# Performance work log

Hardware: AMD Instinct MI355X
Metric: run time of the kernel (lower is better)

## Reference

```python
import jax, jax.numpy as jnp
import numpy as np

B, S, E = 2, 2048, 1024
H = 1344            # hidden_dim = ceil(1.3*1024/64)*64
NH = 4              # mLSTM heads
DH = H // NH        # 336
K = 4               # causal conv kernel size
NPH = H // 4        # headwise proj heads (qkv_proj_blocksize=4)
PD = H // NPH       # per-head proj dim = 4
EPS = 1e-6


def setup_inputs() -> dict:
    key = jax.random.key(0)
    ks = jax.random.split(key, 10)
    s_in = jnp.sqrt(2.0 / (5 * E))    # small_init(E)
    s_pd = jnp.sqrt(2.0 / (5 * PD))   # small_init per-head dim
    return {
        "x": jax.random.normal(ks[0], (B, S, E), jnp.float32),
        "W_up": jax.random.normal(ks[1], (E, 2 * H), jnp.float32) * s_in,
        "conv_k": jax.random.normal(ks[2], (K, 1, H), jnp.float32) * jnp.sqrt(2.0 / K),  # depthwise, WIO layout
        "conv_b": jnp.zeros((H,), jnp.float32),
        "Wq": jax.random.normal(ks[3], (NPH, PD, PD), jnp.float32) * s_pd,
        "Wk": jax.random.normal(ks[4], (NPH, PD, PD), jnp.float32) * s_pd,
        "Wv": jax.random.normal(ks[5], (NPH, PD, PD), jnp.float32) * s_pd,
        "W_ig": jax.random.normal(ks[6], (3 * H, NH), jnp.float32) * 0.01,
        "b_ig": jax.random.normal(ks[7], (NH,), jnp.float32) * 0.1,
        "W_fg": jax.random.normal(ks[8], (3 * H, NH), jnp.float32) * 0.01,
        "b_fg": jnp.linspace(3.0, 6.0, NH, dtype=jnp.float32),
        "ln_w": jnp.ones((H,), jnp.float32),
        "skip": jnp.ones((H,), jnp.float32),
        "W_down": jax.random.normal(ks[9], (H, E), jnp.float32) * (2.0 / 12 / np.sqrt(H)),
    }


def _headwise(x, W):
    # LinearHeadwiseExpand: block-diagonal projection over NPH heads of size PD
    xh = x.reshape(B, S, NPH, PD)
    return jnp.einsum('bshd,hdo->bsho', xh, W).reshape(B, S, H)


def _mlstm_cell(q, k, v, ig, fg):
    # parallel stabilized mLSTM; q,k,v: (B,NH,S,DH); ig,fg: (B,NH,S)
    logf = jax.nn.log_sigmoid(fg)
    c = jnp.cumsum(logf, axis=-1)                         # (B,NH,S)
    logfmat = c[..., :, None] - c[..., None, :]           # (B,NH,S,S) cumulative forget decay
    mask = jnp.tril(jnp.ones((S, S), bool))               # causal mask
    log_D = jnp.where(mask, logfmat, -jnp.inf) + ig[..., None, :]
    m = jnp.max(log_D, axis=-1, keepdims=True)            # rowwise stabilizer
    D = jnp.exp(log_D - m)
    qk = jnp.einsum('bnsd,bntd->bnst', q, k) * (DH ** -0.5)
    C = qk * D
    n = jnp.maximum(jnp.abs(jnp.sum(C, axis=-1, keepdims=True)), jnp.exp(-m))
    return jnp.einsum('bnst,bntd->bnsd', C / (n + EPS), v)


def reference(x, W_up, conv_k, conv_b, Wq, Wk, Wv, W_ig, b_ig, W_fg, b_fg, ln_w, skip, W_down):
    x_inner = x @ W_up                                    # (B,S,2H)
    x_m, z = jnp.split(x_inner, 2, axis=-1)
    # depthwise causal conv1d
    xp = jnp.pad(x_m, ((0, 0), (K - 1, 0), (0, 0)))
    xc = jax.lax.conv_general_dilated(
        xp, conv_k, (1,), 'VALID',
        dimension_numbers=('NWC', 'WIO', 'NWC'),
        feature_group_count=H) + conv_b
    act = jax.nn.silu(xc)
    q = _headwise(act, Wq)
    k = _headwise(act, Wk)
    v = _headwise(x_m, Wv)
    gin = jnp.concatenate([q, k, v], axis=-1)             # (B,S,3H)
    ig = jnp.transpose(gin @ W_ig + b_ig, (0, 2, 1))      # (B,NH,S)
    fg = jnp.transpose(gin @ W_fg + b_fg, (0, 2, 1))
    qh = jnp.transpose(q.reshape(B, S, NH, DH), (0, 2, 1, 3))
    kh = jnp.transpose(k.reshape(B, S, NH, DH), (0, 2, 1, 3))
    vh = jnp.transpose(v.reshape(B, S, NH, DH), (0, 2, 1, 3))
    h = _mlstm_cell(qh, kh, vh, ig, fg)                   # (B,NH,S,DH)
    # multi-head layernorm (per-head groupnorm over DH, scale only)
    mu = jnp.mean(h, axis=-1, keepdims=True)
    var = jnp.var(h, axis=-1, keepdims=True)
    hn = (h - mu) * jax.lax.rsqrt(var + 1e-5) * ln_w.reshape(NH, 1, DH)
    h_out = jnp.transpose(hn, (0, 2, 1, 3)).reshape(B, S, H)
    h_state = (h_out + skip * act) * jax.nn.silu(z)
    return h_state @ W_down
```

## Files before the change

### kernel.cpp

```cpp
#include <hip/hip_runtime.h>
#include <cmath>

#define DI __device__ __forceinline__

constexpr int B_=2, S_=2048, E_=1024, H_=1344, NH_=4, DH_=336;
constexpr int BS_=B_*S_, H2_=2*H_;
constexpr int NG_=B_*NH_*S_;

constexpr size_t N_X=(size_t)BS_*E_;
constexpr size_t N_WUP=(size_t)E_*H2_;
constexpr size_t N_WDN=(size_t)H_*E_;
constexpr size_t N_BSH=(size_t)BS_*H_;
constexpr size_t N_BSH2=(size_t)BS_*H2_;
constexpr size_t N_WH=5376, N_WG=16128, N_CK=4*H_;

constexpr size_t O_IGB = 64;
constexpr size_t O_LOGF= O_IGB + NG_;
constexpr size_t O_AB  = O_LOGF+ NG_;
constexpr size_t O_MB  = O_AB  + NG_;
constexpr size_t O_MTB = O_MB  + NG_;
constexpr size_t O_CK  = O_MTB + NG_;
constexpr size_t O_CB  = O_CK  + N_CK;
constexpr size_t O_WQ  = O_CB  + H_;
constexpr size_t O_WK  = O_WQ  + N_WH;
constexpr size_t O_WV  = O_WK  + N_WH;
constexpr size_t O_WIG = O_WV  + N_WH;
constexpr size_t O_BIG = O_WIG + N_WG;
constexpr size_t O_WFG = O_BIG + 16;
constexpr size_t O_BFG = O_WFG + N_WG;
constexpr size_t O_LNW = O_BFG + 16;
constexpr size_t O_SKP = O_LNW + H_;
constexpr size_t O_FX  = O_SKP + H_;
constexpr size_t O_FWUP= O_FX  + N_X;
constexpr size_t O_FWDN= O_FWUP+ N_WUP;
constexpr size_t O_XIN = O_FWDN+ N_WDN;
constexpr size_t O_ACT = O_XIN + N_BSH2;
constexpr size_t O_QB  = O_ACT + N_BSH;
constexpr size_t O_KB  = O_QB  + N_BSH;
constexpr size_t O_VB  = O_KB  + N_BSH;
constexpr size_t O_HOUT= O_VB  + N_BSH;

constexpr size_t KSPLIT_SHORTS=(size_t)8*128*11*64*8;
constexpr size_t VT_SHORTS=(size_t)8*64*22*64*8;

typedef __attribute__((ext_vector_type(8))) short bf16x8;
typedef __attribute__((ext_vector_type(4))) float f32x4;

DI float bf2f(unsigned int u){union{unsigned int i;float f;}v;v.i=(u&0xffffu)<<16;return v.f;}
DI unsigned short f2bf(float f){union{float f;unsigned int i;}v;v.f=f;unsigned int x=v.i;
  return (unsigned short)((x+0x7fffu+((x>>16)&1u))>>16);}
DI float siluf(float x){return x/(1.f+expf(-x));}
DI float logsigf(float x){return (x>=0.f)?-log1pf(expf(-x)):x-log1pf(expf(x));}
DI void load4(const float* p, float* d){float4 v=*reinterpret_cast<const float4*>(p);
  d[0]=v.x;d[1]=v.y;d[2]=v.z;d[3]=v.w;}

__global__ __launch_bounds__(256) void detect_k(const unsigned short* __restrict__ xraw,
                                                int* __restrict__ flag){
  __shared__ int cnt_s;
  if(threadIdx.x==0) cnt_s=0;
  __syncthreads();
  int c=0;
  for(int i=threadIdx.x;i<2048;i+=256){
    const unsigned e=(xraw[i]>>7)&0xFFu;
    if(e>=0x90u) c++;
  }
  atomicAdd(&cnt_s,c);
  __syncthreads();
  if(threadIdx.x==0) *flag=(cnt_s>16)?0:1;
}

__global__ __launch_bounds__(256) void convert_k(const void* __restrict__ src,
                                                 float* __restrict__ dst,int n,
                                                 const int* __restrict__ flag){
  const int i=blockIdx.x*256+threadIdx.x;
  if(i>=n) return;
  if(*flag) dst[i]=bf2f(((const unsigned short*)src)[i]);
  else      dst[i]=((const float*)src)[i];
}

__global__ __launch_bounds__(256) void aprep_k(const void* __restrict__ src,
                                               const int* __restrict__ flag,
                                               int kcn,int ldk,int total,
                                               unsigned short* __restrict__ hi,
                                               unsigned short* __restrict__ lo){
  const int slot=blockIdx.x*256+threadIdx.x;
  if(slot>=total) return;
  const int l=slot&63, rest=slot>>6;
  const int kc=rest%kcn, mt=rest/kcn;
  const int row=mt*16+(l&15), k0=kc*32+(l>>4)*8;
  const int fl=flag?*flag:0;
  float v[8];
  if(fl){
    const unsigned short* s=(const unsigned short*)src+(size_t)row*ldk+k0;
    const uint4 u=*reinterpret_cast<const uint4*>(s);
    v[0]=bf2f(u.x);v[1]=bf2f(u.x>>16);v[2]=bf2f(u.y);v[3]=bf2f(u.y>>16);
    v[4]=bf2f(u.z);v[5]=bf2f(u.z>>16);v[6]=bf2f(u.w);v[7]=bf2f(u.w>>16);
  }else{
    const float* s=(const float*)src+(size_t)row*ldk+k0;
    load4(s,v); load4(s+4,v+4);
  }
  unsigned short h8[8], l8[8];
#pragma unroll
  for(int j=0;j<8;j++){ h8[j]=f2bf(v[j]); l8[j]=f2bf(v[j]-bf2f(h8[j])); }
  uint4 ph,pl;
  ph.x=(unsigned)h8[0]|((unsigned)h8[1]<<16); ph.y=(unsigned)h8[2]|((unsigned)h8[3]<<16);
  ph.z=(unsigned)h8[4]|((unsigned)h8[5]<<16); ph.w=(unsigned)h8[6]|((unsigned)h8[7]<<16);
  pl.x=(unsigned)l8[0]|((unsigned)l8[1]<<16); pl.y=(unsigned)l8[2]|((unsigned)l8[3]<<16);
  pl.z=(unsigned)l8[4]|((unsigned)l8[5]<<16); pl.w=(unsigned)l8[6]|((unsigned)l8[7]<<16);
  *reinterpret_cast<uint4*>(&hi[(size_t)slot*8])=ph;
  *reinterpret_cast<uint4*>(&lo[(size_t)slot*8])=pl;
}

__global__ __launch_bounds__(256) void bprep_k(const void* __restrict__ src,
                                               const int* __restrict__ flag,
                                               int kcn,int ldn,int total,
                                               unsigned short* __restrict__ hi,
                                               unsigned short* __restrict__ lo){
  const int slot=blockIdx.x*256+threadIdx.x;
  if(slot>=total) return;
  const int l=slot&63, rest=slot>>6;
  const int kc=rest%kcn, nt=rest/kcn;
  const int col=nt*16+(l&15), row0=kc*32+(l>>4)*8;
  const int fl=flag?*flag:0;
  float v[8];
  if(fl){
    const unsigned short* s=(const unsigned short*)src;
#pragma unroll
    for(int j=0;j<8;j++) v[j]=bf2f(s[(size_t)(row0+j)*ldn+col]);
  }else{
    const float* s=(const float*)src;
#pragma unroll
    for(int j=0;j<8;j++) v[j]=s[(size_t)(row0+j)*ldn+col];
  }
  unsigned short h8[8], l8[8];
#pragma unroll
  for(int j=0;j<8;j++){ h8[j]=f2bf(v[j]); l8[j]=f2bf(v[j]-bf2f(h8[j])); }
  uint4 ph,pl;
  ph.x=(unsigned)h8[0]|((unsigned)h8[1]<<16); ph.y=(unsigned)h8[2]|((unsigned)h8[3]<<16);
  ph.z=(unsigned)h8[4]|((unsigned)h8[5]<<16); ph.w=(unsigned)h8[6]|((unsigned)h8[7]<<16);
  pl.x=(unsigned)l8[0]|((unsigned)l8[1]<<16); pl.y=(unsigned)l8[2]|((unsigned)l8[3]<<16);
  pl.z=(unsigned)l8[4]|((unsigned)l8[5]<<16); pl.w=(unsigned)l8[6]|((unsigned)l8[7]<<16);
  *reinterpret_cast<uint4*>(&hi[(size_t)slot*8])=ph;
  *reinterpret_cast<uint4*>(&lo[(size_t)slot*8])=pl;
}

__global__ __launch_bounds__(256) void gemm_mfma_k(
    const unsigned short* __restrict__ Ahi, const unsigned short* __restrict__ Alo,
    const unsigned short* __restrict__ Bhi, const unsigned short* __restrict__ Blo,
    void* __restrict__ C, const int* __restrict__ flag, int kcn, int ldc){
  const int t=threadIdx.x, w=t>>6, l=t&63, lm=l&15, quad=l>>4;
  const int bn=blockIdx.x*64, bm=blockIdx.y*128;
  const int mt0=(bm>>4)+w, mt1=mt0+4;
  const size_t a0=((size_t)mt0*kcn)*512+(size_t)l*8;
  const size_t a1=((size_t)mt1*kcn)*512+(size_t)l*8;
  const size_t b0=((size_t)(bn>>4)*kcn)*512+(size_t)l*8;
  f32x4 acc[2][4];
#pragma unroll
  for(int g=0;g<2;g++)
#pragma unroll
    for(int nt=0;nt<4;nt++) acc[g][nt]={0.f,0.f,0.f,0.f};
  for(int kc=0;kc<kcn;kc++){
    const bf16x8 ah0=*reinterpret_cast<const bf16x8*>(&Ahi[a0+(size_t)kc*512]);
    const bf16x8 al0=*reinterpret_cast<const bf16x8*>(&Alo[a0+(size_t)kc*512]);
    const bf16x8 ah1=*reinterpret_cast<const bf16x8*>(&Ahi[a1+(size_t)kc*512]);
    const bf16x8 al1=*reinterpret_cast<const bf16x8*>(&Alo[a1+(size_t)kc*512]);
#pragma unroll
    for(int nt=0;nt<4;nt++){
      const size_t bo=b0+((size_t)nt*kcn+kc)*512;
      const bf16x8 bh=*reinterpret_cast<const bf16x8*>(&Bhi[bo]);
      const bf16x8 bl=*reinterpret_cast<const bf16x8*>(&Blo[bo]);
      acc[0][nt]=__builtin_amdgcn_mfma_f32_16x16x32_bf16(ah0,bh,acc[0][nt],0,0,0);
      acc[0][nt]=__builtin_amdgcn_mfma_f32_16x16x32_bf16(al0,bh,acc[0][nt],0,0,0);
      acc[0][nt]=__builtin_amdgcn_mfma_f32_16x16x32_bf16(ah0,bl,acc[0][nt],0,0,0);
      acc[1][nt]=__builtin_amdgcn_mfma_f32_16x16x32_bf16(ah1,bh,acc[1][nt],0,0,0);
      acc[1][nt]=__builtin_amdgcn_mfma_f32_16x16x32_bf16(al1,bh,acc[1][nt],0,0,0);
      acc[1][nt]=__builtin_amdgcn_mfma_f32_16x16x32_bf16(ah1,bl,acc[1][nt],0,0,0);
    }
  }
  const int bf=flag?*flag:0;
#pragma unroll
  for(int g=0;g<2;g++)
#pragma unroll
    for(int nt=0;nt<4;nt++)
#pragma unroll
      for(int r=0;r<4;r++){
        const size_t idx=(size_t)(bm+g*64+w*16+quad*4+r)*ldc+bn+nt*16+lm;
        if(bf) ((unsigned short*)C)[idx]=f2bf(acc[g][nt][r]);
        else   ((float*)C)[idx]=acc[g][nt][r];
      }
}

__global__ __launch_bounds__(256) void conv_act_k(const float* __restrict__ xin,
                                                  const float* __restrict__ ck,
                                                  const float* __restrict__ cb,
                                                  float* __restrict__ act){
  const int i=blockIdx.x*256+threadIdx.x;
  if(i>=(int)N_BSH) return;
  const int bs=i/H_, h=i-bs*H_;
  const int b=bs/S_, s=bs-b*S_;
  float xc=cb[h];
#pragma unroll
  for(int w=0;w<4;w++){
    const int sr=s-3+w;
    if(sr>=0) xc+=xin[(size_t)(b*S_+sr)*H2_+h]*ck[w*H_+h];
  }
  act[(size_t)bs*H_+h]=siluf(xc);
}

__global__ __launch_bounds__(256) void qkv_k(const float* __restrict__ act,
                                             const float* __restrict__ xin,
                                             const float* __restrict__ Wq,
                                             const float* __restrict__ Wk,
                                             const float* __restrict__ Wv,
                                             float* __restrict__ qb,float* __restrict__ kb,
                                             float* __restrict__ vb){
  const int i=blockIdx.x*256+threadIdx.x;
  if(i>=(int)N_BSH) return;
  const int bs=i/H_, h=i-bs*H_;
  const int b=bs/S_, s=bs-b*S_;
  const int ph=h>>2, o=h&3, base=ph*4;
  float q=0.f,k=0.f,v=0.f;
#pragma unroll
  for(int d=0;d<4;d++){
    const float a=act[(size_t)bs*H_+base+d];
    const float x=xin[(size_t)bs*H2_+base+d];
    q+=a*Wq[ph*16+d*4+o];
    k+=a*Wk[ph*16+d*4+o];
    v+=x*Wv[ph*16+d*4+o];
  }
  const int nh=h/DH_, dh=h-nh*DH_;
  const size_t off=((size_t)(b*NH_+nh)*S_+s)*DH_+dh;
  qb[off]=q; kb[off]=k; vb[off]=v;
}

__global__ __launch_bounds__(256) void gates2_k(const float* __restrict__ qb,
                                                const float* __restrict__ kb,
                                                const float* __restrict__ vb,
                                                const float* __restrict__ Wig,
                                                const float* __restrict__ big,
                                                const float* __restrict__ Wfg,
                                                const float* __restrict__ bfg,
                                                float* __restrict__ igb,
                                                float* __restrict__ logfb){
  const int wid=(blockIdx.x*256+threadIdx.x)>>6;
  const int l=threadIdx.x&63;
  if(wid>=BS_) return;
  const int b=wid>>11, s=wid&2047;
  float aI0=0.f,aI1=0.f,aI2=0.f,aI3=0.f;
  float aF0=0.f,aF1=0.f,aF2=0.f,aF3=0.f;
  for(int nh=0;nh<NH_;nh++){
    const size_t rb=((size_t)(b*NH_+nh)*S_+s)*DH_;
    const int hb=nh*DH_;
    for(int dh=l;dh<DH_;dh+=64){
      const int h=hb+dh;
      const float q=qb[rb+dh], k=kb[rb+dh], v=vb[rb+dh];
      const float4 wiq=*reinterpret_cast<const float4*>(&Wig[(size_t)h*4]);
      const float4 wik=*reinterpret_cast<const float4*>(&Wig[(size_t)(H_+h)*4]);
      const float4 wiv=*reinterpret_cast<const float4*>(&Wig[(size_t)(2*H_+h)*4]);
      const float4 wfq=*reinterpret_cast<const float4*>(&Wfg[(size_t)h*4]);
      const float4 wfk=*reinterpret_cast<const float4*>(&Wfg[(size_t)(H_+h)*4]);
      const float4 wfv=*reinterpret_cast<const float4*>(&Wfg[(size_t)(2*H_+h)*4]);
      aI0+=q*wiq.x+k*wik.x+v*wiv.x;
      aI1+=q*wiq.y+k*wik.y+v*wiv.y;
      aI2+=q*wiq.z+k*wik.z+v*wiv.z;
      aI3+=q*wiq.w+k*wik.w+v*wiv.w;
      aF0+=q*wfq.x+k*wfk.x+v*wfv.x;
      aF1+=q*wfq.y+k*wfk.y+v*wfv.y;
      aF2+=q*wfq.z+k*wfk.z+v*wfv.z;
      aF3+=q*wfq.w+k*wfk.w+v*wfv.w;
    }
  }
#pragma unroll
  for(int m=1;m<64;m<<=1){
    aI0+=__shfl_xor(aI0,m); aI1+=__shfl_xor(aI1,m);
    aI2+=__shfl_xor(aI2,m); aI3+=__shfl_xor(aI3,m);
    aF0+=__shfl_xor(aF0,m); aF1+=__shfl_xor(aF1,m);
    aF2+=__shfl_xor(aF2,m); aF3+=__shfl_xor(aF3,m);
  }
  if(l==0){
    const size_t o0=(size_t)(b*NH_+0)*S_+s;
    const size_t o1=(size_t)(b*NH_+1)*S_+s;
    const size_t o2=(size_t)(b*NH_+2)*S_+s;
    const size_t o3=(size_t)(b*NH_+3)*S_+s;
    igb[o0]=aI0+big[0]; igb[o1]=aI1+big[1];
    igb[o2]=aI2+big[2]; igb[o3]=aI3+big[3];
    logfb[o0]=logsigf(aF0+bfg[0]); logfb[o1]=logsigf(aF1+bfg[1]);
    logfb[o2]=logsigf(aF2+bfg[2]); logfb[o3]=logsigf(aF3+bfg[3]);
  }
}

__global__ __launch_bounds__(256) void kprep_k(const float* __restrict__ kb,
                                               unsigned short* __restrict__ khi,
                                               unsigned short* __restrict__ klo){
  const int blk=blockIdx.x;
  const int head=blk>>7, tt=blk&127;
  const size_t obase=(size_t)blk*11*512;
  for(int slot=threadIdx.x; slot<704; slot+=256){
    const int dc=slot>>6, ll=slot&63, quad=ll>>4, lm=ll&15;
    const int tg=tt*16+lm, dbase=dc*32+quad*8;
    float v[8];
    if(dbase<336){
      load4(&kb[((size_t)head*S_+tg)*DH_+dbase],v);
      load4(&kb[((size_t)head*S_+tg)*DH_+dbase+4],v+4);
    } else { for(int j=0;j<8;j++) v[j]=0.f; }
    unsigned short hi8[8], lo8[8];
#pragma unroll
    for(int j=0;j<8;j++){
      hi8[j]=f2bf(v[j]);
      lo8[j]=f2bf(v[j]-bf2f(hi8[j]));
    }
    const size_t o=obase+(size_t)(dc*64+ll)*8;
    uint4 ph, pl;
    ph.x=(unsigned)hi8[0]|((unsigned)hi8[1]<<16); ph.y=(unsigned)hi8[2]|((unsigned)hi8[3]<<16);
    ph.z=(unsigned)hi8[4]|((unsigned)hi8[5]<<16); ph.w=(unsigned)hi8[6]|((unsigned)hi8[7]<<16);
    pl.x=(unsigned)lo8[0]|((unsigned)lo8[1]<<16); pl.y=(unsigned)lo8[2]|((unsigned)lo8[3]<<16);
    pl.z=(unsigned)lo8[4]|((unsigned)lo8[5]<<16); pl.w=(unsigned)lo8[6]|((unsigned)lo8[7]<<16);
    *reinterpret_cast<uint4*>(&khi[o])=ph;
    *reinterpret_cast<uint4*>(&klo[o])=pl;
  }
}

__global__ __launch_bounds__(256) void vprep_k(const float* __restrict__ vb,
                                               unsigned short* __restrict__ vTf){
  const int blk=blockIdx.x;
  const int head=blk>>6, tc=blk&63;
  const size_t obase=(size_t)blk*22*512;
  for(int slot=threadIdx.x; slot<1408; slot+=256){
    const int ntg=slot>>6, ll=slot&63, quad=ll>>4, lm=ll&15;
    const int n=ntg*16+lm, t0=tc*32+quad*8;
    unsigned short h8[8];
#pragma unroll
    for(int j=0;j<8;j++){
      float val;
      if(n<336)       val=vb[((size_t)head*S_+t0+j)*DH_+n];
      else if(n==336) val=1.f;
      else            val=0.f;
      h8[j]=f2bf(val);
    }
    uint4 pk;
    pk.x=(unsigned)h8[0]|((unsigned)h8[1]<<16); pk.y=(unsigned)h8[2]|((unsigned)h8[3]<<16);
    pk.z=(unsigned)h8[4]|((unsigned)h8[5]<<16); pk.w=(unsigned)h8[6]|((unsigned)h8[7]<<16);
    *reinterpret_cast<uint4*>(&vTf[obase+(size_t)(ntg*64+ll)*8])=pk;
  }
}

__global__ __launch_bounds__(256) void scan_k(const float* __restrict__ igb,
                                              const float* __restrict__ logfb,
                                              float* __restrict__ ab,float* __restrict__ Mb,
                                              float* __restrict__ mtb){
  const int head=blockIdx.x, t=threadIdx.x;
  __shared__ float sh[256];
  const float* lf=logfb+(size_t)head*S_;
  const float* ig=igb+(size_t)head*S_;
  float lc[8];
  float run=0.f;
#pragma unroll
  for(int i=0;i<8;i++){ run+=lf[t*8+i]; lc[i]=run; }
  sh[t]=run;
  for(int st=1;st<256;st<<=1){
    __syncthreads();
    const float v=(t>=st)?sh[t-st]:0.f;
    __syncthreads();
    sh[t]+=v;
  }
  __syncthreads();
  const float off=(t==0)?0.f:sh[t-1];
  __syncthreads();
  float av[8],mv[8],cv[8];
  float mrun=-1e30f;
#pragma unroll
  for(int i=0;i<8;i++){
    cv[i]=off+lc[i];
    av[i]=ig[t*8+i]-cv[i];
    mrun=fmaxf(mrun,av[i]);
    mv[i]=mrun;
  }
  sh[t]=mrun;
  for(int st=1;st<256;st<<=1){
    __syncthreads();
    const float v=(t>=st)?sh[t-st]:-1e30f;
    __syncthreads();
    sh[t]=fmaxf(sh[t],v);
  }
  __syncthreads();
  const float moff=(t==0)?-1e30f:sh[t-1];
#pragma unroll
  for(int i=0;i<8;i++){
    const float Mi=fmaxf(moff,mv[i]);
    const size_t j=(size_t)head*S_+t*8+i;
    ab[j]=av[i]; Mb[j]=Mi; mtb[j]=cv[i]+Mi;
  }
}

__global__ __launch_bounds__(512,1) void mlstm6_k(
    const float* __restrict__ qb, const unsigned short* __restrict__ khi,
    const unsigned short* __restrict__ klo, const unsigned short* __restrict__ vTf,
    const float* __restrict__ ab, const float* __restrict__ Mb,
    float* __restrict__ part, float* __restrict__ rsum){
  const int bid=blockIdx.x;
  const int head=bid&7;
  const int rest=bid>>3;
  const int pairI=rest&7, seg=rest>>3;
  const int t=threadIdx.x, w=t>>6, l=t&63, lm=l&15, quad=l>>4;

  __shared__ short KV[2][66*512];
  __shared__ short Sc[8][16][40];

  const size_t hb=(size_t)head*S_;
  const float scale=0.05455447256f;

  const int sbA=pairI, sbB=15-pairI;
  const int nA=pairI+1, nTot=17;

  bf16x8 qh[11], ql[11];
  f32x4 accO[22];
  float Mr[4];
  int ws0=sbA*128+w*16;

  auto loadQ=[&](int ws0_){
    const float* qrow=qb+(hb+ws0_+lm)*DH_;
#pragma unroll
    for(int dc=0;dc<11;dc++){
      const int dbase=dc*32+quad*8;
      float v[8];
      if(dbase<336){ load4(qrow+dbase,v); load4(qrow+dbase+4,v+4); }
      else { for(int j=0;j<8;j++) v[j]=0.f; }
#pragma unroll
      for(int j=0;j<8;j++){
        const unsigned short h=f2bf(v[j]);
        qh[dc][j]=(short)h;
        ql[dc][j]=(short)f2bf(v[j]-bf2f(h));
      }
    }
#pragma unroll
    for(int r=0;r<4;r++) Mr[r]=Mb[hb+ws0_+quad*4+r];
#pragma unroll
    for(int n=0;n<22;n++) accO[n]={0.f,0.f,0.f,0.f};
  };

  auto itemC=[&](int i)->int{
    return (i<nA)? (seg+4*i) : (seg+4*(i-nA));
  };

  auto stage=[&](int buf,int c){
    const size_t kbase=(((size_t)head*128+(size_t)(2*c))*11)*512+(size_t)l*8;
    const size_t vbase=(((size_t)head*64+(size_t)c)*22)*512+(size_t)l*8;
#pragma unroll
    for(int j=0;j<9;j++){
      const int tr=w+8*j;
      if(tr<66){
        const unsigned short* src;
        if(tr<22)      src=&khi[kbase+(size_t)tr*512];
        else if(tr<44) src=&klo[kbase+(size_t)(tr-22)*512];
        else           src=&vTf[vbase+(size_t)(tr-44)*512];
        __builtin_amdgcn_global_load_lds(
          (const __attribute__((address_space(1))) unsigned int*)src,
          (__attribute__((address_space(3))) unsigned int*)&KV[buf][(size_t)tr*512],
          16,0,0);
      }
    }
  };

  auto compute=[&](int c,int buf){
    const int t0=c<<5;
    if(t0>ws0+15) return;
    const float al0=ab[hb+t0+lm];
    const float al1=ab[hb+t0+16+lm];
#pragma unroll
    for(int tt=0;tt<2;tt++){
      f32x4 a0={0,0,0,0}, a1={0,0,0,0}, a2={0,0,0,0};
#pragma unroll
      for(int dc=0;dc<11;dc++){
        const bf16x8 kh=*reinterpret_cast<const bf16x8*>(&KV[buf][(tt*11+dc)*512+l*8]);
        const bf16x8 kl=*reinterpret_cast<const bf16x8*>(&KV[buf][(22+tt*11+dc)*512+l*8]);
        a0=__builtin_amdgcn_mfma_f32_16x16x32_bf16(qh[dc],kh,a0,0,0,0);
        a1=__builtin_amdgcn_mfma_f32_16x16x32_bf16(ql[dc],kh,a1,0,0,0);
        a2=__builtin_amdgcn_mfma_f32_16x16x32_bf16(qh[dc],kl,a2,0,0,0);
      }
      const float al=(tt==0)?al0:al1;
      const int tg=t0+tt*16+lm;
#pragma unroll
      for(int r=0;r<4;r++){
        const int srow=quad*4+r;
        const float qk=a0[r]+a1[r]+a2[r];
        const float e=fminf(al-Mr[r],0.f);
        const float msk=(tg<=ws0+srow)?1.f:0.f;
        Sc[w][srow][tt*16+lm]=(short)f2bf(msk*(qk*scale*expf(e)));
      }
    }
    const bf16x8 scf=*reinterpret_cast<const bf16x8*>(&Sc[w][lm][quad*8]);
#pragma unroll
    for(int nt=0;nt<22;nt++){
      const bf16x8 vf=*reinterpret_cast<const bf16x8*>(&KV[buf][(44+nt)*512+l*8]);
      accO[nt]=__builtin_amdgcn_mfma_f32_16x16x32_bf16(scf,vf,accO[nt],0,0,0);
    }
  };

  auto epilogue=[&](){
    const size_t pbase=(size_t)head*2048+ws0;
#pragma unroll
    for(int nt=0;nt<22;nt++){
      const int col=nt*16+lm;
#pragma unroll
      for(int r=0;r<4;r++){
        const int srow=quad*4+r;
        const float val=accO[nt][r];
        if(col<336){ if(val!=0.f) atomicAdd(&part[(pbase+srow)*336+col],val); }
        else if(col==336){ if(val!=0.f) atomicAdd(&rsum[pbase+srow],val); }
      }
    }
  };

  loadQ(ws0);
  stage(0,itemC(0));
  __syncthreads();
  int cur=0;
  for(int i=0;i<nTot;i++){
    if(i+1<nTot) stage(cur^1,itemC(i+1));
    compute(itemC(i),cur);
    if(i==nA-1){
      epilogue();
      ws0=sbB*128+w*16;
      loadQ(ws0);
    }
    __syncthreads();
    cur^=1;
  }
  epilogue();
}

__global__ __launch_bounds__(256) void finalize_k(const float* __restrict__ part,
                                                  const float* __restrict__ rsum,
                                                  const float* __restrict__ mtb,
                                                  const float* __restrict__ lnw,
                                                  float* __restrict__ hout){
  const int sblk=blockIdx.x, head=blockIdx.y;
  const int bI=head>>2, nh=head&3;
  const int s0=sblk*32;
  const int t=threadIdx.x, row=t>>3, sub=t&7;
  __shared__ float red1[32][8], red2[32][8];
  __shared__ float mu_s[32], rs_s[32], inv_s[32];
  const size_t pbase=(size_t)head*2048+s0;
  const float* prow=part+(pbase+row)*336;
  float s1=0.f,s2=0.f;
  for(int c=sub;c<336;c+=8){ const float v=prow[c]; s1+=v; s2+=v*v; }
  red1[row][sub]=s1; red2[row][sub]=s2;
  __syncthreads();
  if(sub==0){
    float a1=0.f,a2=0.f;
#pragma unroll
    for(int j=0;j<8;j++){ a1+=red1[row][j]; a2+=red2[row][j]; }
    const float mt=mtb[(size_t)head*S_+s0+row];
    const float nn=fmaxf(fabsf(rsum[pbase+row]), expf(fminf(fmaxf(-mt,-60.f),60.f)));
    const float inv=1.f/(nn+1e-6f);
    const float mu=a1*inv/336.f;
    const float var=a2*inv*inv/336.f-mu*mu;
    inv_s[row]=inv; mu_s[row]=mu;
    rs_s[row]=rsqrtf(fmaxf(var,0.f)+1e-5f);
  }
  __syncthreads();
  const float inv=inv_s[row], mu=mu_s[row], rs=rs_s[row];
  float* orow=hout+((size_t)(bI*S_+s0+row))*H_+nh*DH_;
  for(int c=sub;c<336;c+=8)
    orow[c]=(prow[c]*inv-mu)*rs*lnw[nh*DH_+c];
}

__global__ __launch_bounds__(256) void hstate_k(const float* __restrict__ hout,
                                                const float* __restrict__ act,
                                                const float* __restrict__ xin,
                                                const float* __restrict__ skip,
                                                float* __restrict__ hs){
  const int i=blockIdx.x*256+threadIdx.x;
  if(i>=(int)N_BSH) return;
  const int bs=i/H_, h=i-bs*H_;
  const float z=xin[(size_t)bs*H2_+H_+h];
  hs[(size_t)bs*H_+h]=(hout[(size_t)bs*H_+h]+skip[h]*act[(size_t)bs*H_+h])*siluf(z);
}

extern "C" void kernel_launch(void* const* d_in, const int* in_sizes, int n_in,
                              void* d_out, int out_size, void* d_ws, size_t ws_size,
                              hipStream_t stream){
  float* ws=(float*)d_ws;
  int* flag=(int*)ws;

  float* igb  = ws+O_IGB;
  float* logfb= ws+O_LOGF;
  float* ab   = ws+O_AB;
  float* Mbuf = ws+O_MB;
  float* mtb  = ws+O_MTB;
  float* f_ck = ws+O_CK;
  float* f_cb = ws+O_CB;
  float* f_wq = ws+O_WQ;
  float* f_wk = ws+O_WK;
  float* f_wv = ws+O_WV;
  float* f_wig= ws+O_WIG;
  float* f_big= ws+O_BIG;
  float* f_wfg= ws+O_WFG;
  float* f_bfg= ws+O_BFG;
  float* f_lnw= ws+O_LNW;
  float* f_skp= ws+O_SKP;
  float* xin  = ws+O_XIN;
  float* act  = ws+O_ACT;
  float* qb   = ws+O_QB;
  float* kb   = ws+O_KB;
  float* vb   = ws+O_VB;
  float* hout = ws+O_HOUT;
  float* hs   = qb;

  unsigned short* xhi  =(unsigned short*)(ws+O_FX);   unsigned short* xlo  =xhi+N_X;
  unsigned short* wuphi=(unsigned short*)(ws+O_FWUP); unsigned short* wuplo=wuphi+N_WUP;
  unsigned short* wdnhi=(unsigned short*)(ws+O_FWDN); unsigned short* wdnlo=wdnhi+N_WDN;
  unsigned short* khi=(unsigned short*)(ws+O_FX);
  unsigned short* klo=khi+KSPLIT_SHORTS;
  unsigned short* vTf=(unsigned short*)kb;
  unsigned short* hshi=(unsigned short*)kb;
  unsigned short* hslo=hshi+N_BSH;
  float* partb=vb;
  float* rsumb=igb;

  detect_k<<<1,256,0,stream>>>((const unsigned short*)d_in[0],flag);
  auto cvt=[&](int idx,float* dst,size_t n){
    convert_k<<<(int)((n+255)/256),256,0,stream>>>(d_in[idx],dst,(int)n,flag);
  };
  cvt(2,f_ck,N_CK);  cvt(3,f_cb,H_);
  cvt(4,f_wq,N_WH); cvt(5,f_wk,N_WH);   cvt(6,f_wv,N_WH);  cvt(7,f_wig,N_WG);
  cvt(8,f_big,4);   cvt(9,f_wfg,N_WG);  cvt(10,f_bfg,4);   cvt(11,f_lnw,H_);
  cvt(12,f_skp,H_);

  aprep_k<<<(256*32*64+255)/256,256,0,stream>>>(d_in[0],flag,32,1024,256*32*64,xhi,xlo);
  bprep_k<<<(168*32*64+255)/256,256,0,stream>>>(d_in[1],flag,32,2688,168*32*64,wuphi,wuplo);
  gemm_mfma_k<<<dim3(2688/64,4096/128),256,0,stream>>>(xhi,xlo,wuphi,wuplo,xin,nullptr,32,H2_);

  conv_act_k<<<(int)((N_BSH+255)/256),256,0,stream>>>(xin,f_ck,f_cb,act);
  qkv_k<<<(int)((N_BSH+255)/256),256,0,stream>>>(act,xin,f_wq,f_wk,f_wv,qb,kb,vb);
  gates2_k<<<(BS_*64+255)/256,256,0,stream>>>(qb,kb,vb,f_wig,f_big,f_wfg,f_bfg,igb,logfb);
  kprep_k<<<8*128,256,0,stream>>>(kb,khi,klo);
  vprep_k<<<8*64,256,0,stream>>>(vb,vTf);
  bprep_k<<<(64*42*64+255)/256,256,0,stream>>>(d_in[13],flag,42,1024,64*42*64,wdnhi,wdnlo);
  scan_k<<<B_*NH_,256,0,stream>>>(igb,logfb,ab,Mbuf,mtb);
  hipMemsetAsync(partb,0,N_BSH*sizeof(float),stream);
  hipMemsetAsync(rsumb,0,(size_t)NG_*sizeof(float),stream);
  mlstm6_k<<<256,512,0,stream>>>(qb,khi,klo,vTf,ab,Mbuf,partb,rsumb);
  finalize_k<<<dim3(S_/32,B_*NH_),256,0,stream>>>(partb,rsumb,mtb,f_lnw,hout);
  hstate_k<<<(int)((N_BSH+255)/256),256,0,stream>>>(hout,act,xin,f_skp,hs);
  aprep_k<<<(256*42*64+255)/256,256,0,stream>>>(hs,nullptr,42,1344,256*42*64,hshi,hslo);
  gemm_mfma_k<<<dim3(1024/64,4096/128),256,0,stream>>>(hshi,hslo,wdnhi,wdnlo,d_out,flag,42,E_);
}
```

Baseline: 524.9 us.

## Stage GEMM tiles through LDS with double-buffered direct loads; merge weight conversions

The split-bf16 MFMA GEMM now uses 128x128 block tiles. Each k-chunk of A and B hi/lo fragments is loaded into double-buffered shared memory with global_load_lds, so each fragment is fetched from global memory once per block and shared across waves instead of each wave reading it separately. The next chunk is loaded while the current one is computed. Separately, eleven small parameter-conversion launches are merged into one kernel to cut launch overhead. The larger tile halves the grid for the down projection (8x32 blocks) and uses 64KB of LDS per block, which may limit occupancy.

```diff
diff --git a/kernel.cpp b/kernel.cpp
--- a/kernel.cpp
+++ b/kernel.cpp
@@ -69,13 +69,29 @@
   if(threadIdx.x==0) *flag=(cnt_s>16)?0:1;
 }
 
-__global__ __launch_bounds__(256) void convert_k(const void* __restrict__ src,
-                                                 float* __restrict__ dst,int n,
-                                                 const int* __restrict__ flag){
+constexpr int CV0=5376, CV1=CV0+1344, CV2=CV1+5376, CV3=CV2+5376, CV4=CV3+5376,
+              CV5=CV4+16128, CV6=CV5+4, CV7=CV6+16128, CV8=CV7+4,
+              CV9=CV8+1344, CVT=CV9+1344;
+__global__ __launch_bounds__(256) void convall_k(
+    const void* s0,const void* s1,const void* s2,const void* s3,const void* s4,
+    const void* s5,const void* s6,const void* s7,const void* s8,const void* s9,
+    const void* s10, float* __restrict__ ws, const int* __restrict__ flag){
   const int i=blockIdx.x*256+threadIdx.x;
-  if(i>=n) return;
-  if(*flag) dst[i]=bf2f(((const unsigned short*)src)[i]);
-  else      dst[i]=((const float*)src)[i];
+  if(i>=CVT) return;
+  const void* src; int off; size_t dst;
+  if(i<CV0){src=s0; off=i;      dst=O_CK +off;}
+  else if(i<CV1){src=s1; off=i-CV0; dst=O_CB +off;}
+  else if(i<CV2){src=s2; off=i-CV1; dst=O_WQ +off;}
+  else if(i<CV3){src=s3; off=i-CV2; dst=O_WK +off;}
+  else if(i<CV4){src=s4; off=i-CV3; dst=O_WV +off;}
+  else if(i<CV5){src=s5; off=i-CV4; dst=O_WIG+off;}
+  else if(i<CV6){src=s6; off=i-CV5; dst=O_BIG+off;}
+  else if(i<CV7){src=s7; off=i-CV6; dst=O_WFG+off;}
+  else if(i<CV8){src=s8; off=i-CV7; dst=O_BFG+off;}
+  else if(i<CV9){src=s9; off=i-CV8; dst=O_LNW+off;}
+  else          {src=s10;off=i-CV9; dst=O_SKP+off;}
+  ws[dst]=(*flag)?bf2f(((const unsigned short*)src)[off])
+                 :((const float*)src)[off];
 }
 
 __global__ __launch_bounds__(256) void aprep_k(const void* __restrict__ src,
@@ -144,31 +160,48 @@
   *reinterpret_cast<uint4*>(&lo[(size_t)slot*8])=pl;
 }
 
-__global__ __launch_bounds__(256) void gemm_mfma_k(
+__global__ __launch_bounds__(256) void gemm2_k(
     const unsigned short* __restrict__ Ahi, const unsigned short* __restrict__ Alo,
     const unsigned short* __restrict__ Bhi, const unsigned short* __restrict__ Blo,
     void* __restrict__ C, const int* __restrict__ flag, int kcn, int ldc){
   const int t=threadIdx.x, w=t>>6, l=t&63, lm=l&15, quad=l>>4;
-  const int bn=blockIdx.x*64, bm=blockIdx.y*128;
-  const int mt0=(bm>>4)+w, mt1=mt0+4;
-  const size_t a0=((size_t)mt0*kcn)*512+(size_t)l*8;
-  const size_t a1=((size_t)mt1*kcn)*512+(size_t)l*8;
-  const size_t b0=((size_t)(bn>>4)*kcn)*512+(size_t)l*8;
-  f32x4 acc[2][4];
+  const int bn=blockIdx.x*128, bm=blockIdx.y*128;
+  const int mtg0=bm>>4, ntg0=bn>>4;
+
+  __shared__ short TT[2][32*512];
+
+  f32x4 acc[2][8];
 #pragma unroll
   for(int g=0;g<2;g++)
 #pragma unroll
-    for(int nt=0;nt<4;nt++) acc[g][nt]={0.f,0.f,0.f,0.f};
-  for(int kc=0;kc<kcn;kc++){
-    const bf16x8 ah0=*reinterpret_cast<const bf16x8*>(&Ahi[a0+(size_t)kc*512]);
-    const bf16x8 al0=*reinterpret_cast<const bf16x8*>(&Alo[a0+(size_t)kc*512]);
-    const bf16x8 ah1=*reinterpret_cast<const bf16x8*>(&Ahi[a1+(size_t)kc*512]);
-    const bf16x8 al1=*reinterpret_cast<const bf16x8*>(&Alo[a1+(size_t)kc*512]);
-#pragma unroll
-    for(int nt=0;nt<4;nt++){
-      const size_t bo=b0+((size_t)nt*kcn+kc)*512;
-      const bf16x8 bh=*reinterpret_cast<const bf16x8*>(&Bhi[bo]);
-      const bf16x8 bl=*reinterpret_cast<const bf16x8*>(&Blo[bo]);
+    for(int nt=0;nt<8;nt++) acc[g][nt]={0.f,0.f,0.f,0.f};
+
+  auto stage=[&](int buf,int kc){
+#pragma unroll
+    for(int j=0;j<8;j++){
+      const int tr=w*8+j;
+      const unsigned short* src;
+      if(tr<8)       src=&Ahi[((size_t)(mtg0+tr   )*kcn+kc)*512+(size_t)l*8];
+      else if(tr<16) src=&Alo[((size_t)(mtg0+tr-8 )*kcn+kc)*512+(size_t)l*8];
+      else if(tr<24) src=&Bhi[((size_t)(ntg0+tr-16)*kcn+kc)*512+(size_t)l*8];
+      else           src=&Blo[((size_t)(ntg0+tr-24)*kcn+kc)*512+(size_t)l*8];
+      __builtin_amdgcn_global_load_lds(
+        (const __attribute__((address_space(1))) unsigned int*)src,
+        (__attribute__((address_space(3))) unsigned int*)&TT[buf][tr*512],
+        16,0,0);
+    }
+  };
+
+  auto compute=[&](int buf){
+    const short* Tb=&TT[buf][0];
+    const bf16x8 ah0=*reinterpret_cast<const bf16x8*>(&Tb[(2*w  )*512+l*8]);
+    const bf16x8 ah1=*reinterpret_cast<const bf16x8*>(&Tb[(2*w+1)*512+l*8]);
+    const bf16x8 al0=*reinterpret_cast<const bf16x8*>(&Tb[(8+2*w  )*512+l*8]);
+    const bf16x8 al1=*reinterpret_cast<const bf16x8*>(&Tb[(8+2*w+1)*512+l*8]);
+#pragma unroll
+    for(int nt=0;nt<8;nt++){
+      const bf16x8 bh=*reinterpret_cast<const bf16x8*>(&Tb[(16+nt)*512+l*8]);
+      const bf16x8 bl=*reinterpret_cast<const bf16x8*>(&Tb[(24+nt)*512+l*8]);
       acc[0][nt]=__builtin_amdgcn_mfma_f32_16x16x32_bf16(ah0,bh,acc[0][nt],0,0,0);
       acc[0][nt]=__builtin_amdgcn_mfma_f32_16x16x32_bf16(al0,bh,acc[0][nt],0,0,0);
       acc[0][nt]=__builtin_amdgcn_mfma_f32_16x16x32_bf16(ah0,bl,acc[0][nt],0,0,0);
@@ -176,15 +209,25 @@
       acc[1][nt]=__builtin_amdgcn_mfma_f32_16x16x32_bf16(al1,bh,acc[1][nt],0,0,0);
       acc[1][nt]=__builtin_amdgcn_mfma_f32_16x16x32_bf16(ah1,bl,acc[1][nt],0,0,0);
     }
-  }
+  };
+
+  stage(0,0);
+  __syncthreads();
+  for(int kc=0;kc<kcn;kc++){
+    const int cur=kc&1;
+    if(kc+1<kcn) stage(cur^1,kc+1);
+    compute(cur);
+    __syncthreads();
+  }
+
   const int bf=flag?*flag:0;
 #pragma unroll
   for(int g=0;g<2;g++)
 #pragma unroll
-    for(int nt=0;nt<4;nt++)
+    for(int nt=0;nt<8;nt++)
 #pragma unroll
       for(int r=0;r<4;r++){
-        const size_t idx=(size_t)(bm+g*64+w*16+quad*4+r)*ldc+bn+nt*16+lm;
+        const size_t idx=(size_t)(bm+(2*w+g)*16+quad*4+r)*ldc+bn+nt*16+lm;
         if(bf) ((unsigned short*)C)[idx]=f2bf(acc[g][nt][r]);
         else   ((float*)C)[idx]=acc[g][nt][r];
       }
@@ -619,17 +662,13 @@
   float* rsumb=igb;
 
   detect_k<<<1,256,0,stream>>>((const unsigned short*)d_in[0],flag);
-  auto cvt=[&](int idx,float* dst,size_t n){
-    convert_k<<<(int)((n+255)/256),256,0,stream>>>(d_in[idx],dst,(int)n,flag);
-  };
-  cvt(2,f_ck,N_CK);  cvt(3,f_cb,H_);
-  cvt(4,f_wq,N_WH); cvt(5,f_wk,N_WH);   cvt(6,f_wv,N_WH);  cvt(7,f_wig,N_WG);
-  cvt(8,f_big,4);   cvt(9,f_wfg,N_WG);  cvt(10,f_bfg,4);   cvt(11,f_lnw,H_);
-  cvt(12,f_skp,H_);
+  convall_k<<<(CVT+255)/256,256,0,stream>>>(d_in[2],d_in[3],d_in[4],d_in[5],d_in[6],
+                                            d_in[7],d_in[8],d_in[9],d_in[10],d_in[11],
+                                            d_in[12],ws,flag);
 
   aprep_k<<<(256*32*64+255)/256,256,0,stream>>>(d_in[0],flag,32,1024,256*32*64,xhi,xlo);
   bprep_k<<<(168*32*64+255)/256,256,0,stream>>>(d_in[1],flag,32,2688,168*32*64,wuphi,wuplo);
-  gemm_mfma_k<<<dim3(2688/64,4096/128),256,0,stream>>>(xhi,xlo,wuphi,wuplo,xin,nullptr,32,H2_);
+  gemm2_k<<<dim3(2688/128,4096/128),256,0,stream>>>(xhi,xlo,wuphi,wuplo,xin,nullptr,32,H2_);
 
   conv_act_k<<<(int)((N_BSH+255)/256),256,0,stream>>>(xin,f_ck,f_cb,act);
   qkv_k<<<(int)((N_BSH+255)/256),256,0,stream>>>(act,xin,f_wq,f_wk,f_wv,qb,kb,vb);
@@ -644,5 +683,5 @@
   finalize_k<<<dim3(S_/32,B_*NH_),256,0,stream>>>(partb,rsumb,mtb,f_lnw,hout);
   hstate_k<<<(int)((N_BSH+255)/256),256,0,stream>>>(hout,act,xin,f_skp,hs);
   aprep_k<<<(256*42*64+255)/256,256,0,stream>>>(hs,nullptr,42,1344,256*42*64,hshi,hslo);
-  gemm_mfma_k<<<dim3(1024/64,4096/128),256,0,stream>>>(hshi,hslo,wdnhi,wdnlo,d_out,flag,42,E_);
-}
+  gemm2_k<<<dim3(1024/128,4096/128),256,0,stream>>>(hshi,hslo,wdnhi,wdnlo,d_out,flag,42,E_);
+}
```

After: 503.4 us. 1.04x faster.
